# Kernel optimization log

Measured on AMD Instinct MI355X. Metric: run time of the kernel, lower is better.

The kernel has to match this reference:

```python
import jax, jax.numpy as jnp
import numpy as np

B, S, D = 1, 4096, 1024
H, HKV, HD = 16, 4, 64          # q heads, kv heads, head dim
ROPE_THETA = 1e6


def setup_inputs() -> dict:
    key = jax.random.key(0)
    k1, k2, k3 = jax.random.split(key, 3)
    x = jax.random.normal(k1, (B, S, D), dtype=jnp.float32)
    # deterministic RoPE tables: pos_cis = exp(i * t * theta^{-2j/hd})
    inv_freq = 1.0 / (ROPE_THETA ** (np.arange(0, HD, 2, dtype=np.float32) / HD))  # [HD//2]
    ang = np.arange(S, dtype=np.float32)[:, None] * inv_freq[None, :]              # [S, HD//2]
    pos_cos = jnp.asarray(np.cos(ang), dtype=jnp.float32)
    pos_sin = jnp.asarray(np.sin(ang), dtype=jnp.float32)
    w_qkv = jax.random.normal(k2, (D, (H + 2 * HKV) * HD), dtype=jnp.float32) * 0.02
    w_o = jax.random.normal(k3, (H * HD, D), dtype=jnp.float32) * 0.02
    return {"x": x, "pos_cos": pos_cos, "pos_sin": pos_sin, "w_qkv": w_qkv, "w_o": w_o}


def _rope(t, pos_cos, pos_sin):
    # t: [B, S, h, HD]; complex pairs are consecutive elements on last dim
    te, to = t[..., 0::2], t[..., 1::2]
    cos = pos_cos[None, :, None, :]
    sin = pos_sin[None, :, None, :]
    oe = te * cos - to * sin
    oo = te * sin + to * cos
    return jnp.stack([oe, oo], axis=-1).reshape(t.shape)


def reference(x, pos_cos, pos_sin, w_qkv, w_o):
    qkv = jnp.einsum("bsd,de->bse", x, w_qkv)  # fused QKV projection
    q = qkv[..., : H * HD].reshape(B, S, H, HD)
    k = qkv[..., H * HD : (H + HKV) * HD].reshape(B, S, HKV, HD)
    v = qkv[..., (H + HKV) * HD :].reshape(B, S, HKV, HD)
    q = _rope(q, pos_cos, pos_sin)
    k = _rope(k, pos_cos, pos_sin)
    # GQA: repeat kv heads to match q heads
    n_rep = H // HKV
    k = jnp.repeat(k, n_rep, axis=2)  # [B, S, H, HD]
    v = jnp.repeat(v, n_rep, axis=2)
    scale = 1.0 / jnp.sqrt(jnp.float32(HD))
    scores = jnp.einsum("bqhd,bkhd->bhqk", q, k) * scale  # [B, H, S, S]
    causal = jnp.tril(jnp.ones((S, S), dtype=bool))
    scores = jnp.where(causal[None, None], scores, jnp.float32(-1e9))
    attn = jax.nn.softmax(scores, axis=-1)
    out = jnp.einsum("bhqk,bkhd->bqhd", attn, v).reshape(B, S, H * HD)
    return jnp.einsum("bse,ed->bsd", out, w_o)
```

## Files before the change

### kernel.cpp

```cpp
#include <hip/hip_runtime.h>

#define S_LEN 4096
#define DMODEL 1024
#define NH 16
#define NKV 4
#define HDIM 64
#define NQKV 1536

typedef __attribute__((ext_vector_type(8))) short bfrag8;
typedef __attribute__((ext_vector_type(4))) float f32x4_t;

__device__ __forceinline__ unsigned short f2bf(float f) {
  unsigned int u = __builtin_bit_cast(unsigned int, f);
  return (unsigned short)((u + 0x7fffu + ((u >> 16) & 1u)) >> 16);
}

__device__ __forceinline__ unsigned int cvtpk_bf16(float lo, float hi) {
  unsigned int r;
  asm("v_cvt_pk_bf16_f32 %0, %1, %2" : "=v"(r) : "v"(lo), "v"(hi));
  return r;
}

__device__ __forceinline__ float fexp2(float x) {
  float r;
  asm("v_exp_f32 %0, %1" : "=v"(r) : "v"(x));
  return r;
}

__device__ __forceinline__ float fmax3(float a, float b, float c) {
  float r;
  asm("v_max3_f32 %0, %1, %2, %3" : "=v"(r) : "v"(a), "v"(b), "v"(c));
  return r;
}

typedef __attribute__((address_space(3))) unsigned char lds_uc;
typedef const __attribute__((address_space(1))) unsigned char glob_uc;
__device__ __forceinline__ void gl16(const void* g, void* l) {
  __builtin_amdgcn_global_load_lds((glob_uc*)g, (lds_uc*)l, 16, 0, 0);
}

__global__ void preprocess(const float* __restrict__ x, const float* __restrict__ wqkv,
                           const float* __restrict__ wo,
                           unsigned short* __restrict__ xb, unsigned short* __restrict__ wqkvT,
                           unsigned short* __restrict__ woT) {
  __shared__ float tile[32][33];
  int b = blockIdx.x;
  int t = threadIdx.x;
  if (b < 4096) {
    int idx = (b * 256 + t) * 4;
    float4 v = *reinterpret_cast<const float4*>(x + idx);
    xb[idx + 0] = f2bf(v.x);
    xb[idx + 1] = f2bf(v.y);
    xb[idx + 2] = f2bf(v.z);
    xb[idx + 3] = f2bf(v.w);
    return;
  }
  int tx = t & 31, ty = t >> 5;
  const float* in;
  unsigned short* out;
  int ldin, ldout, c0, r0;
  if (b < 4096 + 1536) {
    int id = b - 4096;
    c0 = (id % 48) * 32;
    r0 = (id / 48) * 32;
    in = wqkv; out = wqkvT; ldin = NQKV; ldout = DMODEL;
  } else {
    int id = b - 4096 - 1536;
    c0 = (id & 31) * 32;
    r0 = (id >> 5) * 32;
    in = wo; out = woT; ldin = DMODEL; ldout = DMODEL;
  }
  for (int i = 0; i < 4; ++i) {
    int r = r0 + ty + i * 8;
    tile[ty + i * 8][tx] = in[(size_t)r * ldin + c0 + tx];
  }
  __syncthreads();
  for (int i = 0; i < 4; ++i) {
    int c = c0 + ty + i * 8;
    out[(size_t)c * ldout + r0 + tx] = f2bf(tile[tx][ty + i * 8]);
  }
}

__global__ void rope_vt(const float* __restrict__ qkv,
                        const float* __restrict__ pcos, const float* __restrict__ psin,
                        unsigned short* __restrict__ Qh, unsigned short* __restrict__ Kh,
                        unsigned short* __restrict__ Vt) {
  int b = blockIdx.x;
  int t = threadIdx.x;
  if (b < 4096) {
    const float SCL = 0.125f * 1.44269504f;
    int s = b;
    const float* row = qkv + (size_t)s * NQKV;
    for (int p = t; p < 640; p += 256) {
      int i = p & 31;
      float c = pcos[s * 32 + i], sn = psin[s * 32 + i];
      if (p < 512) {
        int h = p >> 5;
        float te = row[h * 64 + 2 * i], to = row[h * 64 + 2 * i + 1];
        size_t base = ((size_t)h * S_LEN + s) * 64;
        Qh[base + 2 * i]     = f2bf((te * c - to * sn) * SCL);
        Qh[base + 2 * i + 1] = f2bf((te * sn + to * c) * SCL);
      } else {
        int hk = (p - 512) >> 5;
        float te = row[1024 + hk * 64 + 2 * i], to = row[1024 + hk * 64 + 2 * i + 1];
        size_t base = ((size_t)hk * S_LEN + s) * 64;
        Kh[base + 2 * i]     = f2bf(te * c - to * sn);
        Kh[base + 2 * i + 1] = f2bf(te * sn + to * c);
      }
    }
    return;
  }
  __shared__ float tile[32][33];
  int id = b - 4096;
  int dt = id & 1;
  int st = (id >> 1) & 127;
  int hk = id >> 8;
  int tx = t & 31, ty = t >> 5;
  const float* inb = qkv + 1280 + hk * 64 + dt * 32;
  unsigned short* outb = Vt + (size_t)hk * HDIM * S_LEN + (size_t)dt * 32 * S_LEN;
  int s0 = st * 32;
  for (int i = 0; i < 4; ++i) {
    int r = s0 + ty + i * 8;
    tile[ty + i * 8][tx] = inb[(size_t)r * NQKV + tx];
  }
  __syncthreads();
  for (int i = 0; i < 4; ++i) {
    int d = ty + i * 8;
    outb[(size_t)d * S_LEN + s0 + tx] = f2bf(tile[tx][d]);
  }
}

__global__ __launch_bounds__(256) void gemm_bf16(
    const unsigned short* __restrict__ A,
    const unsigned short* __restrict__ Bt,
    float* __restrict__ C, int M, int N, int K) {
  __shared__ __align__(16) unsigned short As[64 * 64];
  __shared__ __align__(16) unsigned short Bs[128 * 64];
  int m0 = blockIdx.x * 64, n0 = blockIdx.y * 128;
  int t = threadIdx.x, lane = t & 63, wid = t >> 6;
  int wm = (wid >> 1) * 32, wn = (wid & 1) * 64;
  int fr = lane & 15, kb = lane >> 4;
  int srow = t >> 3, scol = (t & 7) * 8;
  const unsigned short* Ag0 = A + (size_t)(m0 + srow) * K + scol;
  const unsigned short* Ag1 = A + (size_t)(m0 + 32 + srow) * K + scol;
  const unsigned short* Bg0 = Bt + (size_t)(n0 + srow) * K + scol;
  const unsigned short* Bg1 = Bt + (size_t)(n0 + 32 + srow) * K + scol;
  const unsigned short* Bg2 = Bt + (size_t)(n0 + 64 + srow) * K + scol;
  const unsigned short* Bg3 = Bt + (size_t)(n0 + 96 + srow) * K + scol;
  char* AsD0 = (char*)As + wid * 1024;
  char* AsD1 = (char*)As + 4096 + wid * 1024;
  char* BsD0 = (char*)Bs + wid * 1024;
  char* BsD1 = (char*)Bs + 4096 + wid * 1024;
  char* BsD2 = (char*)Bs + 8192 + wid * 1024;
  char* BsD3 = (char*)Bs + 12288 + wid * 1024;

  f32x4_t acc[2][4];
#pragma unroll
  for (int r = 0; r < 2; ++r)
#pragma unroll
    for (int c = 0; c < 4; ++c) acc[r][c] = (f32x4_t){0.f, 0.f, 0.f, 0.f};

  for (int k0 = 0; k0 < K; k0 += 64) {
    __syncthreads();
    gl16(Ag0 + k0, AsD0);
    gl16(Ag1 + k0, AsD1);
    gl16(Bg0 + k0, BsD0);
    gl16(Bg1 + k0, BsD1);
    gl16(Bg2 + k0, BsD2);
    gl16(Bg3 + k0, BsD3);
    __syncthreads();
    bfrag8 af[2][2], bfr[4][2];
#pragma unroll
    for (int rb = 0; rb < 2; ++rb)
#pragma unroll
      for (int h = 0; h < 2; ++h)
        af[rb][h] = *reinterpret_cast<const bfrag8*>(&As[(wm + rb * 16 + fr) * 64 + h * 32 + kb * 8]);
#pragma unroll
    for (int cb = 0; cb < 4; ++cb)
#pragma unroll
      for (int h = 0; h < 2; ++h)
        bfr[cb][h] = *reinterpret_cast<const bfrag8*>(&Bs[(wn + cb * 16 + fr) * 64 + h * 32 + kb * 8]);
#pragma unroll
    for (int rb = 0; rb < 2; ++rb)
#pragma unroll
      for (int cb = 0; cb < 4; ++cb) {
        acc[rb][cb] = __builtin_amdgcn_mfma_f32_16x16x32_bf16(af[rb][0], bfr[cb][0], acc[rb][cb], 0, 0, 0);
        acc[rb][cb] = __builtin_amdgcn_mfma_f32_16x16x32_bf16(af[rb][1], bfr[cb][1], acc[rb][cb], 0, 0, 0);
      }
  }
  int rowg = (lane >> 4) * 4, colg = lane & 15;
#pragma unroll
  for (int rb = 0; rb < 2; ++rb)
#pragma unroll
    for (int cb = 0; cb < 4; ++cb)
#pragma unroll
      for (int j = 0; j < 4; ++j) {
        int r = m0 + wm + rb * 16 + rowg + j;
        int c = n0 + wn + cb * 16 + colg;
        C[(size_t)r * N + c] = acc[rb][cb][j];
      }
}

__global__ __launch_bounds__(256) void flash_attn(
    const unsigned short* __restrict__ Qh,
    const unsigned short* __restrict__ Kh,
    const unsigned short* __restrict__ Vt,
    unsigned short* __restrict__ aout) {
  __shared__ __align__(16) char SMEM[18432];
  int bid = blockIdx.x;
  int hk = bid & 3;
  int head = hk * 4 + ((bid >> 2) & 3);
  int qt = 127 - (bid >> 4);
  int qrow0 = qt * 32;
  int t = threadIdx.x, lane = t & 63, wid = t >> 6;
  int fr = lane & 15, kb = lane >> 4, rloc = kb * 4;
  char* Pw = SMEM + wid * 4096;
  int swz = (fr & 7) << 4;

  const unsigned short* Qbase = Qh + ((size_t)head * S_LEN + qrow0) * 64;
  bfrag8 qf[2][2];
  qf[0][0] = *reinterpret_cast<const bfrag8*>(Qbase + fr * 64 + kb * 8);
  qf[0][1] = *reinterpret_cast<const bfrag8*>(Qbase + fr * 64 + 32 + kb * 8);
  qf[1][0] = *reinterpret_cast<const bfrag8*>(Qbase + (16 + fr) * 64 + kb * 8);
  qf[1][1] = *reinterpret_cast<const bfrag8*>(Qbase + (16 + fr) * 64 + 32 + kb * 8);

  const unsigned short* Kt = Kh + (size_t)hk * S_LEN * 64;
  const unsigned short* Vb = Vt + (size_t)hk * 64 * S_LEN;
  int koff = fr * 64 + kb * 8;
  int voff = fr * S_LEN + kb * 8;

  float m_r[2] = {-1e30f, -1e30f}, l_r[2] = {0.f, 0.f};
  f32x4_t acc[2][4];
#pragma unroll
  for (int g = 0; g < 2; ++g)
#pragma unroll
    for (int dt = 0; dt < 4; ++dt) acc[g][dt] = (f32x4_t){0.f, 0.f, 0.f, 0.f};

  int ntt = (qrow0 + 95) / 64;
  int nf = (qrow0 >= 63) ? ((qrow0 - 63) / 64 + 1) : 0;
  int c0 = (wid * ntt) >> 2, c1 = ((wid + 1) * ntt) >> 2;

  if (c0 < c1) {
    bfrag8 kf[4][2];
    {
      const unsigned short* K0 = Kt + c0 * 64 * 64 + koff;
#pragma unroll
      for (int ct = 0; ct < 4; ++ct) {
        kf[ct][0] = *reinterpret_cast<const bfrag8*>(K0 + ct * 1024);
        kf[ct][1] = *reinterpret_cast<const bfrag8*>(K0 + ct * 1024 + 32);
      }
    }
    for (int kt = c0; kt < c1; ++kt) {
      int kv0 = kt * 64;
      const unsigned short* Vtile = Vb + kv0 + voff;
      bfrag8 vf[2][4];
#pragma unroll
      for (int hh = 0; hh < 2; ++hh)
#pragma unroll
        for (int dt = 0; dt < 4; ++dt)
          vf[hh][dt] = *reinterpret_cast<const bfrag8*>(Vtile + dt * 16 * S_LEN + hh * 32);
      __builtin_amdgcn_sched_barrier(0);
      f32x4_t sc[2][4];
      __builtin_amdgcn_s_setprio(1);
#pragma unroll
      for (int ct = 0; ct < 4; ++ct) {
        f32x4_t z0 = (f32x4_t){0.f, 0.f, 0.f, 0.f};
        z0 = __builtin_amdgcn_mfma_f32_16x16x32_bf16(kf[ct][0], qf[0][0], z0, 0, 0, 0);
        sc[0][ct] = __builtin_amdgcn_mfma_f32_16x16x32_bf16(kf[ct][1], qf[0][1], z0, 0, 0, 0);
        f32x4_t z1 = (f32x4_t){0.f, 0.f, 0.f, 0.f};
        z1 = __builtin_amdgcn_mfma_f32_16x16x32_bf16(kf[ct][0], qf[1][0], z1, 0, 0, 0);
        sc[1][ct] = __builtin_amdgcn_mfma_f32_16x16x32_bf16(kf[ct][1], qf[1][1], z1, 0, 0, 0);
      }
      __builtin_amdgcn_s_setprio(0);
      if (kt + 1 < c1) {
        const unsigned short* Kn = Kt + (kv0 + 64) * 64 + koff;
#pragma unroll
        for (int ct = 0; ct < 4; ++ct) {
          kf[ct][0] = *reinterpret_cast<const bfrag8*>(Kn + ct * 1024);
          kf[ct][1] = *reinterpret_cast<const bfrag8*>(Kn + ct * 1024 + 32);
        }
      }
      __builtin_amdgcn_sched_barrier(0);
      if (kt >= nf) {
#pragma unroll
        for (int g = 0; g < 2; ++g) {
          int grow = qrow0 + g * 16 + fr;
#pragma unroll
          for (int ct = 0; ct < 4; ++ct)
#pragma unroll
            for (int j = 0; j < 4; ++j)
              sc[g][ct][j] = ((kv0 + ct * 16 + kb * 4 + j) <= grow) ? sc[g][ct][j] : -1e30f;
        }
      }
      float pmax[2];
#pragma unroll
      for (int g = 0; g < 2; ++g) {
        float pm = fmax3(sc[g][0][0], sc[g][0][1], sc[g][0][2]);
        pm = fmax3(pm, sc[g][0][3], sc[g][1][0]);
        pm = fmax3(pm, sc[g][1][1], sc[g][1][2]);
        pm = fmax3(pm, sc[g][1][3], sc[g][2][0]);
        pm = fmax3(pm, sc[g][2][1], sc[g][2][2]);
        pm = fmax3(pm, sc[g][2][3], sc[g][3][0]);
        pm = fmax3(pm, sc[g][3][1], sc[g][3][2]);
        pm = fmaxf(pm, sc[g][3][3]);
        pm = fmaxf(pm, __shfl_xor(pm, 16));
        pmax[g] = fmaxf(pm, __shfl_xor(pm, 32));
      }
      bool need = (pmax[0] > m_r[0] + 8.0f) || (pmax[1] > m_r[1] + 8.0f);
      if (__any(need)) {
#pragma unroll
        for (int g = 0; g < 2; ++g) {
          float mnew = fmaxf(m_r[g], pmax[g]);
          float a = fexp2(m_r[g] - mnew);
          l_r[g] *= a;
          m_r[g] = mnew;
#pragma unroll
          for (int j = 0; j < 4; ++j) {
            float aj = __shfl(a, rloc + j);
#pragma unroll
            for (int dt = 0; dt < 4; ++dt) acc[g][dt][j] *= aj;
          }
        }
      }
#pragma unroll
      for (int g = 0; g < 2; ++g) {
        float st[4];
#pragma unroll
        for (int ct = 0; ct < 4; ++ct) {
          float p0 = fexp2(sc[g][ct][0] - m_r[g]);
          float p1 = fexp2(sc[g][ct][1] - m_r[g]);
          float p2 = fexp2(sc[g][ct][2] - m_r[g]);
          float p3 = fexp2(sc[g][ct][3] - m_r[g]);
          sc[g][ct][0] = p0; sc[g][ct][1] = p1; sc[g][ct][2] = p2; sc[g][ct][3] = p3;
          st[ct] = (p0 + p1) + (p2 + p3);
        }
        l_r[g] += (st[0] + st[1]) + (st[2] + st[3]);
      }
#pragma unroll
      for (int g = 0; g < 2; ++g)
#pragma unroll
        for (int ct = 0; ct < 4; ++ct) {
          unsigned int u01 = cvtpk_bf16(sc[g][ct][0], sc[g][ct][1]);
          unsigned int u23 = cvtpk_bf16(sc[g][ct][2], sc[g][ct][3]);
          unsigned long long w = ((unsigned long long)u23 << 32) | u01;
          *reinterpret_cast<unsigned long long*>(
              Pw + (g * 16 + fr) * 128 + ((ct * 32 + kb * 8) ^ swz)) = w;
        }
      __builtin_amdgcn_s_setprio(1);
#pragma unroll
      for (int hh = 0; hh < 2; ++hh) {
        bfrag8 pa0 = *reinterpret_cast<const bfrag8*>(Pw + fr * 128 + ((hh * 64 + kb * 16) ^ swz));
        bfrag8 pa1 = *reinterpret_cast<const bfrag8*>(Pw + (16 + fr) * 128 + ((hh * 64 + kb * 16) ^ swz));
#pragma unroll
        for (int dt = 0; dt < 4; ++dt) {
          acc[0][dt] = __builtin_amdgcn_mfma_f32_16x16x32_bf16(pa0, vf[hh][dt], acc[0][dt], 0, 0, 0);
          acc[1][dt] = __builtin_amdgcn_mfma_f32_16x16x32_bf16(pa1, vf[hh][dt], acc[1][dt], 0, 0, 0);
        }
      }
      __builtin_amdgcn_s_setprio(0);
    }
  }

  float* stgA = (float*)SMEM;
  float* stgB = (float*)(SMEM + 9216);
  __syncthreads();
  if (wid == 1 || wid == 3) {
    float* R = (wid == 1) ? stgA : stgB;
#pragma unroll
    for (int g = 0; g < 2; ++g) {
#pragma unroll
      for (int dt = 0; dt < 4; ++dt)
#pragma unroll
        for (int j = 0; j < 4; ++j)
          R[(g * 16 + dt * 4 + j) * 64 + lane] = acc[g][dt][j];
      R[(32 + g * 2) * 64 + lane] = m_r[g];
      R[(33 + g * 2) * 64 + lane] = l_r[g];
    }
  }
  __syncthreads();
  if (wid == 0 || wid == 2) {
    float* R = (wid == 0) ? stgA : stgB;
#pragma unroll
    for (int g = 0; g < 2; ++g) {
      float mo = R[(32 + g * 2) * 64 + lane], lo = R[(33 + g * 2) * 64 + lane];
      float mm = fmaxf(m_r[g], mo);
      float ca = fexp2(m_r[g] - mm), cb = fexp2(mo - mm);
      l_r[g] = l_r[g] * ca + lo * cb;
      m_r[g] = mm;
#pragma unroll
      for (int j = 0; j < 4; ++j) {
        float caj = __shfl(ca, rloc + j);
        float cbj = __shfl(cb, rloc + j);
#pragma unroll
        for (int dt = 0; dt < 4; ++dt)
          acc[g][dt][j] = acc[g][dt][j] * caj + R[(g * 16 + dt * 4 + j) * 64 + lane] * cbj;
      }
    }
    if (wid == 2) {
#pragma unroll
      for (int g = 0; g < 2; ++g) {
#pragma unroll
        for (int dt = 0; dt < 4; ++dt)
#pragma unroll
          for (int j = 0; j < 4; ++j)
            stgB[(g * 16 + dt * 4 + j) * 64 + lane] = acc[g][dt][j];
        stgB[(32 + g * 2) * 64 + lane] = m_r[g];
        stgB[(33 + g * 2) * 64 + lane] = l_r[g];
      }
    }
  }
  __syncthreads();
  if (wid == 0) {
#pragma unroll
    for (int g = 0; g < 2; ++g) {
      float mo = stgB[(32 + g * 2) * 64 + lane], lo = stgB[(33 + g * 2) * 64 + lane];
      float mm = fmaxf(m_r[g], mo);
      float ca = fexp2(m_r[g] - mm), cb = fexp2(mo - mm);
      l_r[g] = l_r[g] * ca + lo * cb;
#pragma unroll
      for (int j = 0; j < 4; ++j) {
        float caj = __shfl(ca, rloc + j);
        float cbj = __shfl(cb, rloc + j);
#pragma unroll
        for (int dt = 0; dt < 4; ++dt)
          acc[g][dt][j] = acc[g][dt][j] * caj + stgB[(g * 16 + dt * 4 + j) * 64 + lane] * cbj;
      }
    }
#pragma unroll
    for (int g = 0; g < 2; ++g) {
      l_r[g] += __shfl_xor(l_r[g], 16);
      l_r[g] += __shfl_xor(l_r[g], 32);
    }
#pragma unroll
    for (int g = 0; g < 2; ++g)
#pragma unroll
      for (int j = 0; j < 4; ++j) {
        float lj = __shfl(l_r[g], rloc + j);
        float inv = 1.0f / lj;
        int grow = qrow0 + g * 16 + rloc + j;
#pragma unroll
        for (int dt = 0; dt < 4; ++dt)
          aout[(size_t)grow * (NH * HDIM) + head * 64 + dt * 16 + fr] = f2bf(acc[g][dt][j] * inv);
      }
  }
}

extern "C" void kernel_launch(void* const* d_in, const int* in_sizes, int n_in,
                              void* d_out, int out_size, void* d_ws, size_t ws_size,
                              hipStream_t stream) {
  const float* x    = (const float*)d_in[0];
  const float* pcos = (const float*)d_in[1];
  const float* psin = (const float*)d_in[2];
  const float* wqkv = (const float*)d_in[3];
  const float* wo   = (const float*)d_in[4];
  float* out = (float*)d_out;

  char* ws = (char*)d_ws;
  unsigned short* xb    = (unsigned short*)ws;  ws += (size_t)S_LEN * DMODEL * 2;
  unsigned short* wqkvT = (unsigned short*)ws;  ws += (size_t)NQKV * DMODEL * 2;
  unsigned short* woT   = (unsigned short*)ws;  ws += (size_t)DMODEL * DMODEL * 2;
  float*          qkv   = (float*)ws;           ws += (size_t)S_LEN * NQKV * 4;
  unsigned short* Qh    = (unsigned short*)ws;  ws += (size_t)NH * S_LEN * HDIM * 2;
  unsigned short* Kh    = (unsigned short*)ws;  ws += (size_t)NKV * S_LEN * HDIM * 2;
  unsigned short* Vt    = (unsigned short*)ws;  ws += (size_t)NKV * HDIM * S_LEN * 2;
  unsigned short* aoutb = (unsigned short*)ws;  ws += (size_t)S_LEN * NH * HDIM * 2;

  preprocess<<<dim3(4096 + 1536 + 1024), 256, 0, stream>>>(x, wqkv, wo, xb, wqkvT, woT);
  gemm_bf16<<<dim3(S_LEN / 64, NQKV / 128), 256, 0, stream>>>(xb, wqkvT, qkv, S_LEN, NQKV, DMODEL);
  rope_vt<<<dim3(4096 + 1024), 256, 0, stream>>>(qkv, pcos, psin, Qh, Kh, Vt);
  flash_attn<<<dim3(2048), 256, 0, stream>>>(Qh, Kh, Vt, aoutb);
  gemm_bf16<<<dim3(S_LEN / 64, DMODEL / 128), 256, 0, stream>>>(aoutb, woT, out, S_LEN, DMODEL, DMODEL);
}
```

Baseline: 189.5 us.

## Fuse RoPE, scaling and V transpose into QKV GEMM epilogue

Replaces the separate QKV GEMM plus rope_vt kernel with one GEMM whose epilogue applies RoPE via lane shuffles, scales Q, converts to bf16, and writes K/Q head-major and V transposed directly. This removes the fp32 qkv intermediate (a 24MB write and read) and one kernel launch. In exchange, the epilogue does scattered 2-byte stores and per-element cos/sin loads, which may coalesce poorly.

```diff
diff --git a/kernel.cpp b/kernel.cpp
--- a/kernel.cpp
+++ b/kernel.cpp
@@ -81,52 +81,107 @@
   }
 }
 
-__global__ void rope_vt(const float* __restrict__ qkv,
-                        const float* __restrict__ pcos, const float* __restrict__ psin,
-                        unsigned short* __restrict__ Qh, unsigned short* __restrict__ Kh,
-                        unsigned short* __restrict__ Vt) {
-  int b = blockIdx.x;
-  int t = threadIdx.x;
-  if (b < 4096) {
-    const float SCL = 0.125f * 1.44269504f;
-    int s = b;
-    const float* row = qkv + (size_t)s * NQKV;
-    for (int p = t; p < 640; p += 256) {
-      int i = p & 31;
-      float c = pcos[s * 32 + i], sn = psin[s * 32 + i];
-      if (p < 512) {
-        int h = p >> 5;
-        float te = row[h * 64 + 2 * i], to = row[h * 64 + 2 * i + 1];
-        size_t base = ((size_t)h * S_LEN + s) * 64;
-        Qh[base + 2 * i]     = f2bf((te * c - to * sn) * SCL);
-        Qh[base + 2 * i + 1] = f2bf((te * sn + to * c) * SCL);
-      } else {
-        int hk = (p - 512) >> 5;
-        float te = row[1024 + hk * 64 + 2 * i], to = row[1024 + hk * 64 + 2 * i + 1];
-        size_t base = ((size_t)hk * S_LEN + s) * 64;
-        Kh[base + 2 * i]     = f2bf(te * c - to * sn);
-        Kh[base + 2 * i + 1] = f2bf(te * sn + to * c);
-      }
-    }
-    return;
-  }
-  __shared__ float tile[32][33];
-  int id = b - 4096;
-  int dt = id & 1;
-  int st = (id >> 1) & 127;
-  int hk = id >> 8;
-  int tx = t & 31, ty = t >> 5;
-  const float* inb = qkv + 1280 + hk * 64 + dt * 32;
-  unsigned short* outb = Vt + (size_t)hk * HDIM * S_LEN + (size_t)dt * 32 * S_LEN;
-  int s0 = st * 32;
-  for (int i = 0; i < 4; ++i) {
-    int r = s0 + ty + i * 8;
-    tile[ty + i * 8][tx] = inb[(size_t)r * NQKV + tx];
-  }
-  __syncthreads();
-  for (int i = 0; i < 4; ++i) {
-    int d = ty + i * 8;
-    outb[(size_t)d * S_LEN + s0 + tx] = f2bf(tile[tx][d]);
+__global__ __launch_bounds__(256) void gemm_qkv_rope(
+    const unsigned short* __restrict__ A,
+    const unsigned short* __restrict__ Bt,
+    const float* __restrict__ pcos, const float* __restrict__ psin,
+    unsigned short* __restrict__ Qh,
+    unsigned short* __restrict__ Kh,
+    unsigned short* __restrict__ Vt) {
+  const int K = DMODEL;
+  __shared__ __align__(16) unsigned short As[64 * 64];
+  __shared__ __align__(16) unsigned short Bs[128 * 64];
+  int m0 = blockIdx.x * 64, n0 = blockIdx.y * 128;
+  int t = threadIdx.x, lane = t & 63, wid = t >> 6;
+  int wm = (wid >> 1) * 32, wn = (wid & 1) * 64;
+  int fr = lane & 15, kb = lane >> 4;
+  int srow = t >> 3, scol = (t & 7) * 8;
+  const unsigned short* Ag0 = A + (size_t)(m0 + srow) * K + scol;
+  const unsigned short* Ag1 = A + (size_t)(m0 + 32 + srow) * K + scol;
+  const unsigned short* Bg0 = Bt + (size_t)(n0 + srow) * K + scol;
+  const unsigned short* Bg1 = Bt + (size_t)(n0 + 32 + srow) * K + scol;
+  const unsigned short* Bg2 = Bt + (size_t)(n0 + 64 + srow) * K + scol;
+  const unsigned short* Bg3 = Bt + (size_t)(n0 + 96 + srow) * K + scol;
+  char* AsD0 = (char*)As + wid * 1024;
+  char* AsD1 = (char*)As + 4096 + wid * 1024;
+  char* BsD0 = (char*)Bs + wid * 1024;
+  char* BsD1 = (char*)Bs + 4096 + wid * 1024;
+  char* BsD2 = (char*)Bs + 8192 + wid * 1024;
+  char* BsD3 = (char*)Bs + 12288 + wid * 1024;
+
+  f32x4_t acc[2][4];
+#pragma unroll
+  for (int r = 0; r < 2; ++r)
+#pragma unroll
+    for (int c = 0; c < 4; ++c) acc[r][c] = (f32x4_t){0.f, 0.f, 0.f, 0.f};
+
+  for (int k0 = 0; k0 < K; k0 += 64) {
+    __syncthreads();
+    gl16(Ag0 + k0, AsD0);
+    gl16(Ag1 + k0, AsD1);
+    gl16(Bg0 + k0, BsD0);
+    gl16(Bg1 + k0, BsD1);
+    gl16(Bg2 + k0, BsD2);
+    gl16(Bg3 + k0, BsD3);
+    __syncthreads();
+    bfrag8 af[2][2], bfr[4][2];
+#pragma unroll
+    for (int rb = 0; rb < 2; ++rb)
+#pragma unroll
+      for (int h = 0; h < 2; ++h)
+        af[rb][h] = *reinterpret_cast<const bfrag8*>(&As[(wm + rb * 16 + fr) * 64 + h * 32 + kb * 8]);
+#pragma unroll
+    for (int cb = 0; cb < 4; ++cb)
+#pragma unroll
+      for (int h = 0; h < 2; ++h)
+        bfr[cb][h] = *reinterpret_cast<const bfrag8*>(&Bs[(wn + cb * 16 + fr) * 64 + h * 32 + kb * 8]);
+#pragma unroll
+    for (int rb = 0; rb < 2; ++rb)
+#pragma unroll
+      for (int cb = 0; cb < 4; ++cb) {
+        acc[rb][cb] = __builtin_amdgcn_mfma_f32_16x16x32_bf16(af[rb][0], bfr[cb][0], acc[rb][cb], 0, 0, 0);
+        acc[rb][cb] = __builtin_amdgcn_mfma_f32_16x16x32_bf16(af[rb][1], bfr[cb][1], acc[rb][cb], 0, 0, 0);
+      }
+  }
+
+  const float SCL = 0.125f * 1.44269504f;
+  int rowg = (lane >> 4) * 4, colg = lane & 15;
+  int hsec = (n0 + wn) >> 6;
+  int odd = lane & 1;
+  if (hsec < NH + NKV) {
+    unsigned short* dst = (hsec < NH) ? (Qh + (size_t)hsec * S_LEN * 64)
+                                      : (Kh + (size_t)(hsec - NH) * S_LEN * 64);
+    float scale = (hsec < NH) ? SCL : 1.0f;
+#pragma unroll
+    for (int rb = 0; rb < 2; ++rb)
+#pragma unroll
+      for (int cb = 0; cb < 4; ++cb) {
+        int d = cb * 16 + colg;
+        int i = d >> 1;
+#pragma unroll
+        for (int j = 0; j < 4; ++j) {
+          int r = m0 + wm + rb * 16 + rowg + j;
+          float v = acc[rb][cb][j];
+          float p = __shfl_xor(v, 1);
+          float co = pcos[r * 32 + i], si = psin[r * 32 + i];
+          float o = odd ? (p * si + v * co) : (v * co - p * si);
+          dst[(size_t)r * 64 + d] = f2bf(o * scale);
+        }
+      }
+  } else {
+    int hk = hsec - NH - NKV;
+    unsigned short* dst = Vt + (size_t)hk * HDIM * S_LEN;
+#pragma unroll
+    for (int rb = 0; rb < 2; ++rb)
+#pragma unroll
+      for (int cb = 0; cb < 4; ++cb) {
+        int d = cb * 16 + colg;
+        int r0 = m0 + wm + rb * 16 + rowg;
+        unsigned int u01 = (unsigned int)f2bf(acc[rb][cb][0]) | ((unsigned int)f2bf(acc[rb][cb][1]) << 16);
+        unsigned int u23 = (unsigned int)f2bf(acc[rb][cb][2]) | ((unsigned int)f2bf(acc[rb][cb][3]) << 16);
+        unsigned long long w = ((unsigned long long)u23 << 32) | u01;
+        *reinterpret_cast<unsigned long long*>(&dst[(size_t)d * S_LEN + r0]) = w;
+      }
   }
 }
 
@@ -459,15 +514,13 @@
   unsigned short* xb    = (unsigned short*)ws;  ws += (size_t)S_LEN * DMODEL * 2;
   unsigned short* wqkvT = (unsigned short*)ws;  ws += (size_t)NQKV * DMODEL * 2;
   unsigned short* woT   = (unsigned short*)ws;  ws += (size_t)DMODEL * DMODEL * 2;
-  float*          qkv   = (float*)ws;           ws += (size_t)S_LEN * NQKV * 4;
   unsigned short* Qh    = (unsigned short*)ws;  ws += (size_t)NH * S_LEN * HDIM * 2;
   unsigned short* Kh    = (unsigned short*)ws;  ws += (size_t)NKV * S_LEN * HDIM * 2;
   unsigned short* Vt    = (unsigned short*)ws;  ws += (size_t)NKV * HDIM * S_LEN * 2;
   unsigned short* aoutb = (unsigned short*)ws;  ws += (size_t)S_LEN * NH * HDIM * 2;
 
   preprocess<<<dim3(4096 + 1536 + 1024), 256, 0, stream>>>(x, wqkv, wo, xb, wqkvT, woT);
-  gemm_bf16<<<dim3(S_LEN / 64, NQKV / 128), 256, 0, stream>>>(xb, wqkvT, qkv, S_LEN, NQKV, DMODEL);
-  rope_vt<<<dim3(4096 + 1024), 256, 0, stream>>>(qkv, pcos, psin, Qh, Kh, Vt);
+  gemm_qkv_rope<<<dim3(S_LEN / 64, NQKV / 128), 256, 0, stream>>>(xb, wqkvT, pcos, psin, Qh, Kh, Vt);
   flash_attn<<<dim3(2048), 256, 0, stream>>>(Qh, Kh, Vt, aoutb);
   gemm_bf16<<<dim3(S_LEN / 64, DMODEL / 128), 256, 0, stream>>>(aoutb, woT, out, S_LEN, DMODEL, DMODEL);
 }
```

New measurement: 182.2 us, median of 2. 3.9% less time.
